# Kernel tuning notes

Hardware: AMD Instinct MI355X
Metric: run time of the kernel (lower is better)

Reference implementation:

```python
import jax, jax.numpy as jnp
import numpy as np

N_AUTHOR, N_FOS, N_INST, N_PAPER = 100000, 30000, 8000, 200000
D_IN, D_OUT = 128, 128
# (name, n_src, n_dst, n_edges)
RELS = [("aff", N_AUTHOR, N_INST, 150000), ("ita", N_INST, N_AUTHOR, 150000),
        ("writes", N_AUTHOR, N_PAPER, 500000), ("pta", N_PAPER, N_AUTHOR, 500000),
        ("cites", N_PAPER, N_PAPER, 1000000), ("topic", N_PAPER, N_FOS, 500000),
        ("ftp", N_FOS, N_PAPER, 500000)]
NODE_SIZES = {"author": N_AUTHOR, "fos": N_FOS, "inst": N_INST, "paper": N_PAPER}


def setup_inputs() -> dict:
    key = jax.random.key(0)
    ks = iter(jax.random.split(key, 64))
    inp = {}
    for nt, n in NODE_SIZES.items():
        inp[f"x_{nt}"] = jax.random.normal(next(ks), (n, D_IN), jnp.float32)
    for name, ns, nd, e in RELS:
        inp[f"src_{name}"] = jax.random.randint(next(ks), (e,), 0, ns, jnp.int64)
        inp[f"dst_{name}"] = jax.random.randint(next(ks), (e,), 0, nd, jnp.int64)
    w_scale = 1.0 / np.sqrt(D_IN)
    for nt in NODE_SIZES:
        inp[f"W_root_{nt}"] = jax.random.uniform(next(ks), (D_IN, D_OUT), jnp.float32, -w_scale, w_scale)
        inp[f"b_root_{nt}"] = jax.random.uniform(next(ks), (D_OUT,), jnp.float32, -w_scale, w_scale)
    for name, _, _, _ in RELS:
        inp[f"W_{name}"] = jax.random.uniform(next(ks), (D_IN, D_OUT), jnp.float32, -w_scale, w_scale)
    return inp


def _mean_agg(x_src, src, dst, n_dst):
    # gather source features along edges, mean-reduce into destinations
    msg = x_src[src]                                             # [E, D_IN]
    s = jax.ops.segment_sum(msg, dst, num_segments=n_dst)        # [n_dst, D_IN]
    cnt = jax.ops.segment_sum(jnp.ones_like(dst, dtype=x_src.dtype), dst, num_segments=n_dst)
    return s / jnp.maximum(cnt, 1.0)[:, None]                    # isolated nodes -> 0


def reference(x_author, x_fos, x_inst, x_paper,
              W_root_author, b_root_author, W_root_fos, b_root_fos,
              W_root_inst, b_root_inst, W_root_paper, b_root_paper,
              W_aff, W_ita, W_writes, W_pta, W_cites, W_topic, W_ftp,
              src_aff, dst_aff, src_ita, dst_ita, src_writes, dst_writes,
              src_pta, dst_pta, src_cites, dst_cites, src_topic, dst_topic,
              src_ftp, dst_ftp):
    # root (self) transforms
    out_author = x_author @ W_root_author + b_root_author
    out_fos = x_fos @ W_root_fos + b_root_fos
    out_inst = x_inst @ W_root_inst + b_root_inst
    out_paper = x_paper @ W_root_paper + b_root_paper
    # per-relation aggregate -> linear -> accumulate into destination type
    out_inst = out_inst + _mean_agg(x_author, src_aff, dst_aff, N_INST) @ W_aff
    out_author = out_author + _mean_agg(x_inst, src_ita, dst_ita, N_AUTHOR) @ W_ita
    out_paper = out_paper + _mean_agg(x_author, src_writes, dst_writes, N_PAPER) @ W_writes
    out_author = out_author + _mean_agg(x_paper, src_pta, dst_pta, N_AUTHOR) @ W_pta
    out_paper = out_paper + _mean_agg(x_paper, src_cites, dst_cites, N_PAPER) @ W_cites
    out_fos = out_fos + _mean_agg(x_paper, src_topic, dst_topic, N_FOS) @ W_topic
    out_paper = out_paper + _mean_agg(x_fos, src_ftp, dst_ftp, N_PAPER) @ W_ftp
    # concatenate per-type outputs (author, fos, inst, paper) along node axis
    return jnp.concatenate([out_author, out_fos, out_inst, out_paper], axis=0)
```

## Files before the change

kernel.cpp:

```cpp
#include <hip/hip_runtime.h>

#define N_AUTHOR 100000
#define N_FOS    30000
#define N_INST   8000
#define N_PAPER  200000
#define NCNT     838000
#define ETOT     3300000

typedef __attribute__((ext_vector_type(8))) short short8v;
typedef __attribute__((ext_vector_type(4))) float float4v;

__device__ __forceinline__ unsigned short f2bf(float f) {
  unsigned u = __float_as_uint(f);
  u = u + 0x7fffu + ((u >> 16) & 1u);
  return (unsigned short)(u >> 16);
}
#define BF2F(s) __uint_as_float(((unsigned)(unsigned short)(s)) << 16)

__device__ __forceinline__ void acc8(float4v& x, float4v& y, short8v h) {
  x[0] += BF2F(h[0]); x[1] += BF2F(h[1]); x[2] += BF2F(h[2]); x[3] += BF2F(h[3]);
  y[0] += BF2F(h[4]); y[1] += BF2F(h[5]); y[2] += BF2F(h[6]); y[3] += BF2F(h[7]);
}

__device__ __forceinline__ short8v pack8(float4v a, float4v b) {
  short8v h;
  h[0] = (short)f2bf(a[0]); h[1] = (short)f2bf(a[1]);
  h[2] = (short)f2bf(a[2]); h[3] = (short)f2bf(a[3]);
  h[4] = (short)f2bf(b[0]); h[5] = (short)f2bf(b[1]);
  h[6] = (short)f2bf(b[2]); h[7] = (short)f2bf(b[3]);
  return h;
}

#define O_CNT    0
#define O_OFFS   3352000
#define O_CURSOR 6704000
#define O_BTOT   10056000
#define O_CSR    10060096
#define O_WT     23260096
#define XB_AUTHOR 23620544
#define XB_FOS    49220544
#define XB_INST   56900544
#define XB_PAPER  58948544
#define WS_NEED_BF 110148544ULL

struct RelTab { const int* src; const int* dst; int E; int base; };
struct Rels { RelTab r[7]; };
struct WPtrs { const float* w[11]; };
struct XCvt { const float* x; unsigned short* xb; int n8; };

__global__ void prep(WPtrs P, unsigned short* __restrict__ wt,
                     int* __restrict__ cnt, XCvt x0, XCvt x1, XCvt x2, XCvt x3,
                     Rels R, int doX) {
  int gsz = gridDim.x * blockDim.x;
  int gtid = blockIdx.x * blockDim.x + threadIdx.x;
  for (int i = gtid; i < 11 * 16384; i += gsz) {
    int mat = i >> 14, rem = i & 16383;
    int k = rem >> 7, n = rem & 127;
    wt[mat * 16384 + n * 128 + k] = f2bf(P.w[mat][rem]);
  }
  if (doX) {
    XCvt xc[4] = {x0, x1, x2, x3};
    #pragma unroll
    for (int a = 0; a < 4; ++a) {
      const float* xp = xc[a].x;
      short8v* xbp = (short8v*)xc[a].xb;
      int n8 = xc[a].n8;
      for (int i = gtid; i < n8; i += gsz) {
        float4v v0 = *(const float4v*)(xp + (size_t)i * 8);
        float4v v1 = *(const float4v*)(xp + (size_t)i * 8 + 4);
        xbp[i] = pack8(v0, v1);
      }
    }
  }
  #pragma unroll
  for (int rr = 0; rr < 7; ++rr) {
    const int* dst = R.r[rr].dst;
    int E = R.r[rr].E, base = R.r[rr].base;
    for (int e = gtid; e < E; e += gsz) atomicAdd(&cnt[base + dst[e]], 1);
  }
}

__global__ void scan1(const int* __restrict__ cnt, int* __restrict__ offs,
                      int* __restrict__ btot, int n) {
  __shared__ int sh[256];
  int tid = threadIdx.x;
  int base = blockIdx.x * 2048 + tid * 8;
  int v[8]; int s = 0;
  #pragma unroll
  for (int i = 0; i < 8; ++i) { v[i] = (base + i < n) ? cnt[base + i] : 0; s += v[i]; }
  sh[tid] = s; __syncthreads();
  for (int off = 1; off < 256; off <<= 1) {
    int t = (tid >= off) ? sh[tid - off] : 0;
    __syncthreads();
    sh[tid] += t;
    __syncthreads();
  }
  int excl = sh[tid] - s;
  if (tid == 255) btot[blockIdx.x] = sh[255];
  int run = excl;
  #pragma unroll
  for (int i = 0; i < 8; ++i) { if (base + i < n) offs[base + i] = run; run += v[i]; }
}

__global__ void scan23(int* __restrict__ offs, int* __restrict__ cursor,
                       const int* __restrict__ btot, int nb, int n) {
  __shared__ int sh[512];
  int tid = threadIdx.x;
  int v = (tid < nb) ? btot[tid] : 0;
  sh[tid] = v; __syncthreads();
  for (int off = 1; off < 512; off <<= 1) {
    int t = (tid >= off) ? sh[tid - off] : 0;
    __syncthreads();
    sh[tid] += t;
    __syncthreads();
  }
  int excl = sh[tid] - v;
  __syncthreads();
  sh[tid] = excl;
  __syncthreads();
  int gsz = gridDim.x * 512;
  for (int idx = blockIdx.x * 512 + tid; idx < n; idx += gsz) {
    int val = offs[idx] + sh[idx >> 11];
    offs[idx] = val;
    cursor[idx] = val;
  }
}

__global__ void fill_k(Rels R, int* __restrict__ cursor, int* __restrict__ csr) {
  int gsz = gridDim.x * blockDim.x;
  int gtid = blockIdx.x * blockDim.x + threadIdx.x;
  #pragma unroll
  for (int rr = 0; rr < 7; ++rr) {
    const int* src = R.r[rr].src;
    const int* dst = R.r[rr].dst;
    int E = R.r[rr].E, base = R.r[rr].base;
    for (int e = gtid; e < E; e += gsz) {
      int p = atomicAdd(&cursor[base + dst[e]], 1);
      __builtin_nontemporal_store(src[e], &csr[p]);
    }
  }
}

template <int NSRC>
__global__ __launch_bounds__(256, 4) void fused_t(
    const unsigned short* __restrict__ x0, const unsigned short* __restrict__ x1,
    const unsigned short* __restrict__ x2, const unsigned short* __restrict__ x3,
    const unsigned short* __restrict__ w0, const unsigned short* __restrict__ w1,
    const unsigned short* __restrict__ w2, const unsigned short* __restrict__ w3,
    int b1, int b2, int b3,
    const int* __restrict__ offs, const int* __restrict__ cnt,
    const int* __restrict__ csr,
    const float* __restrict__ bias, float* __restrict__ out, int n) {
  const int lane = threadIdx.x & 63;
  const int wv = threadIdx.x >> 6;
  const int rb = blockIdx.x * 64 + wv * 16;
  int ar = rb + (lane & 15); if (ar >= n) ar = n - 1;
  const int ch = lane >> 4;
  const int cw = ch * 8;

  const unsigned short* xs[4] = {x0, x1, x2, x3};
  const unsigned short* wsp[4] = {w0, w1, w2, w3};
  const int bases[4] = {0, b1, b2, b3};

  float4v acc[8];
  #pragma unroll
  for (int i = 0; i < 8; ++i) acc[i] = (float4v)0.0f;

  #pragma unroll
  for (int kb = 0; kb < NSRC; ++kb) {
    short8v af[4];
    if (kb == 0) {
      const unsigned short* rp = xs[0] + (size_t)ar * 128 + cw;
      #pragma unroll
      for (int ks = 0; ks < 4; ++ks)
        af[ks] = *(const short8v*)(rp + ks * 32);
    } else {
      int gd = bases[kb] + ar;
      int st = offs[gd];
      int deg = cnt[gd];
      const unsigned short* xb = xs[kb];
      float4v a0[4], a1[4];
      #pragma unroll
      for (int ks = 0; ks < 4; ++ks) { a0[ks] = (float4v)0.f; a1[ks] = (float4v)0.f; }
      int j = 0;
      for (; j + 2 <= deg; j += 2) {
        int s0 = csr[st + j], s1 = csr[st + j + 1];
        const unsigned short* p0 = xb + (size_t)s0 * 128 + cw;
        const unsigned short* p1 = xb + (size_t)s1 * 128 + cw;
        #pragma unroll
        for (int ks = 0; ks < 4; ++ks) {
          short8v h0 = *(const short8v*)(p0 + ks * 32);
          short8v h1 = *(const short8v*)(p1 + ks * 32);
          acc8(a0[ks], a1[ks], h0);
          acc8(a0[ks], a1[ks], h1);
        }
      }
      if (j < deg) {
        int s0 = csr[st + j];
        const unsigned short* p0 = xb + (size_t)s0 * 128 + cw;
        #pragma unroll
        for (int ks = 0; ks < 4; ++ks) {
          short8v h0 = *(const short8v*)(p0 + ks * 32);
          acc8(a0[ks], a1[ks], h0);
        }
      }
      float sc = 1.0f / (float)((deg > 0) ? deg : 1);
      #pragma unroll
      for (int ks = 0; ks < 4; ++ks)
        af[ks] = pack8(a0[ks] * sc, a1[ks] * sc);
    }
    const unsigned short* wb = wsp[kb] + (size_t)(lane & 15) * 128 + cw;
    #pragma unroll
    for (int ct = 0; ct < 8; ++ct) {
      short8v bfr[4];
      #pragma unroll
      for (int ks = 0; ks < 4; ++ks)
        bfr[ks] = *(const short8v*)(wb + ct * 2048 + ks * 32);
      #pragma unroll
      for (int ks = 0; ks < 4; ++ks)
        acc[ct] = __builtin_amdgcn_mfma_f32_16x16x32_bf16(af[ks], bfr[ks], acc[ct], 0, 0, 0);
    }
  }
  #pragma unroll
  for (int ct = 0; ct < 8; ++ct) {
    #pragma unroll
    for (int i = 0; i < 4; ++i) {
      int g = rb + (lane >> 4) * 4 + i;
      if (g < n) {
        int col = ct * 16 + (lane & 15);
        out[(size_t)g * 128 + col] = acc[ct][i] + bias[col];
      }
    }
  }
}

typedef float4v f4;
__global__ __launch_bounds__(256, 4) void fb_gemm(
    const float* __restrict__ x0, const float* __restrict__ x1,
    const float* __restrict__ x2, const float* __restrict__ x3,
    const unsigned short* __restrict__ w0, const unsigned short* __restrict__ w1,
    const unsigned short* __restrict__ w2, const unsigned short* __restrict__ w3,
    int nsrc, int b1, int b2, int b3,
    const int* __restrict__ offs, const int* __restrict__ cnt,
    const int* __restrict__ csr,
    const float* __restrict__ bias, float* __restrict__ out, int n) {
  const int lane = threadIdx.x & 63;
  const int wv = threadIdx.x >> 6;
  const int rb = blockIdx.x * 64 + wv * 16;
  int ar = rb + (lane & 15); if (ar >= n) ar = n - 1;
  const int ch = lane >> 4, cw = ch * 8;
  const float* xs[4] = {x0, x1, x2, x3};
  const unsigned short* wsp[4] = {w0, w1, w2, w3};
  const int bases[4] = {0, b1, b2, b3};
  float4v acc[8];
  #pragma unroll
  for (int i = 0; i < 8; ++i) acc[i] = (float4v)0.0f;
  for (int kb = 0; kb < nsrc; ++kb) {
    short8v af[4];
    const float* xb = xs[kb];
    if (kb == 0) {
      const float* rp = xb + (size_t)ar * 128 + cw;
      #pragma unroll
      for (int ks = 0; ks < 4; ++ks) {
        f4 u = *(const f4*)(rp + ks * 32);
        f4 v = *(const f4*)(rp + ks * 32 + 4);
        af[ks] = pack8(u, v);
      }
    } else {
      int gd = bases[kb] + ar;
      int st = offs[gd];
      int deg = cnt[gd];
      f4 a0[4], a1[4];
      #pragma unroll
      for (int ks = 0; ks < 4; ++ks) { a0[ks] = (f4)0.f; a1[ks] = (f4)0.f; }
      for (int j = 0; j < deg; ++j) {
        int s0 = csr[st + j];
        const float* p0 = xb + (size_t)s0 * 128 + cw;
        #pragma unroll
        for (int ks = 0; ks < 4; ++ks) {
          a0[ks] += *(const f4*)(p0 + ks * 32);
          a1[ks] += *(const f4*)(p0 + ks * 32 + 4);
        }
      }
      float sc = 1.0f / (float)((deg > 0) ? deg : 1);
      #pragma unroll
      for (int ks = 0; ks < 4; ++ks)
        af[ks] = pack8(a0[ks] * sc, a1[ks] * sc);
    }
    const unsigned short* wb = wsp[kb] + (size_t)(lane & 15) * 128 + cw;
    #pragma unroll
    for (int ct = 0; ct < 8; ++ct) {
      short8v bfr[4];
      #pragma unroll
      for (int ks = 0; ks < 4; ++ks)
        bfr[ks] = *(const short8v*)(wb + ct * 2048 + ks * 32);
      #pragma unroll
      for (int ks = 0; ks < 4; ++ks)
        acc[ct] = __builtin_amdgcn_mfma_f32_16x16x32_bf16(af[ks], bfr[ks], acc[ct], 0, 0, 0);
    }
  }
  #pragma unroll
  for (int ct = 0; ct < 8; ++ct) {
    #pragma unroll
    for (int i = 0; i < 4; ++i) {
      int g = rb + (lane >> 4) * 4 + i;
      if (g < n) {
        int col = ct * 16 + (lane & 15);
        out[(size_t)g * 128 + col] = acc[ct][i] + bias[col];
      }
    }
  }
}

extern "C" void kernel_launch(void* const* d_in, const int* in_sizes, int n_in,
                              void* d_out, int out_size, void* d_ws, size_t ws_size,
                              hipStream_t stream) {
  const float* x_author = (const float*)d_in[0];
  const float* x_fos    = (const float*)d_in[1];
  const float* x_inst   = (const float*)d_in[2];
  const float* x_paper  = (const float*)d_in[3];

  Rels R;
  const int E[7]  = {150000, 150000, 500000, 500000, 1000000, 500000, 500000};
  const int ND[7] = {N_INST, N_AUTHOR, N_PAPER, N_AUTHOR, N_PAPER, N_FOS, N_PAPER};
  int base = 0;
  for (int r = 0; r < 7; ++r) {
    R.r[r].src = (const int*)d_in[4 + 2 * r];
    R.r[r].dst = (const int*)d_in[5 + 2 * r];
    R.r[r].E = E[r];
    R.r[r].base = base;
    base += ND[r];
  }

  char* ws = (char*)d_ws;
  int* cnt    = (int*)(ws + O_CNT);
  int* offs   = (int*)(ws + O_OFFS);
  int* cursor = (int*)(ws + O_CURSOR);
  int* btot   = (int*)(ws + O_BTOT);
  int* csr    = (int*)(ws + O_CSR);
  unsigned short* wt = (unsigned short*)(ws + O_WT);
  unsigned short* xbA = (unsigned short*)(ws + XB_AUTHOR);
  unsigned short* xbF = (unsigned short*)(ws + XB_FOS);
  unsigned short* xbI = (unsigned short*)(ws + XB_INST);
  unsigned short* xbP = (unsigned short*)(ws + XB_PAPER);

  const int useBF = (ws_size >= WS_NEED_BF) ? 1 : 0;

  WPtrs WP;
  WP.w[0] = (const float*)d_in[18];
  WP.w[1] = (const float*)d_in[20];
  WP.w[2] = (const float*)d_in[22];
  WP.w[3] = (const float*)d_in[24];
  for (int r = 0; r < 7; ++r) WP.w[4 + r] = (const float*)d_in[26 + r];

  XCvt xcA = {x_author, xbA, N_AUTHOR * 16};
  XCvt xcF = {x_fos,    xbF, N_FOS * 16};
  XCvt xcI = {x_inst,   xbI, N_INST * 16};
  XCvt xcP = {x_paper,  xbP, N_PAPER * 16};

  hipMemsetAsync(cnt, 0, (size_t)NCNT * 4, stream);
  prep<<<2048, 256, 0, stream>>>(WP, wt, cnt, xcA, xcF, xcI, xcP, R, useBF);
  scan1<<<410, 256, 0, stream>>>(cnt, offs, btot, NCNT);
  scan23<<<1024, 512, 0, stream>>>(offs, cursor, btot, 410, NCNT);
  fill_k<<<2048, 256, 0, stream>>>(R, cursor, csr);

  float* out = (float*)d_out;
  const int B_AFF = 0, B_ITA = 8000, B_WRITES = 108000, B_PTA = 308000,
            B_CITES = 408000, B_TOPIC = 608000, B_FTP = 638000;

  const int NB_AUTHOR = (N_AUTHOR + 63) / 64;
  const int NB_FOS    = (N_FOS + 63) / 64;
  const int NB_INST   = (N_INST + 63) / 64;
  const int NB_PAPER  = (N_PAPER + 63) / 64;

  float* outA = out;
  float* outF = out + (size_t)100000 * 128;
  float* outI = out + (size_t)130000 * 128;
  float* outP = out + (size_t)138000 * 128;
  const float* bA = (const float*)d_in[19];
  const float* bF = (const float*)d_in[21];
  const float* bI = (const float*)d_in[23];
  const float* bP = (const float*)d_in[25];

  if (useBF) {
    fused_t<3><<<NB_AUTHOR, 256, 0, stream>>>(
        xbA, xbI, xbP, nullptr,
        wt + 0 * 16384, wt + 5 * 16384, wt + 7 * 16384, nullptr,
        B_ITA, B_PTA, 0, offs, cnt, csr, bA, outA, N_AUTHOR);
    fused_t<2><<<NB_FOS, 256, 0, stream>>>(
        xbF, xbP, nullptr, nullptr,
        wt + 1 * 16384, wt + 9 * 16384, nullptr, nullptr,
        B_TOPIC, 0, 0, offs, cnt, csr, bF, outF, N_FOS);
    fused_t<2><<<NB_INST, 256, 0, stream>>>(
        xbI, xbA, nullptr, nullptr,
        wt + 2 * 16384, wt + 4 * 16384, nullptr, nullptr,
        B_AFF, 0, 0, offs, cnt, csr, bI, outI, N_INST);
    fused_t<4><<<NB_PAPER, 256, 0, stream>>>(
        xbP, xbA, xbP, xbF,
        wt + 3 * 16384, wt + 6 * 16384, wt + 8 * 16384, wt + 10 * 16384,
        B_WRITES, B_CITES, B_FTP, offs, cnt, csr, bP, outP, N_PAPER);
  } else {
    fb_gemm<<<NB_AUTHOR, 256, 0, stream>>>(
        x_author, x_inst, x_paper, nullptr,
        wt + 0 * 16384, wt + 5 * 16384, wt + 7 * 16384, nullptr,
        3, B_ITA, B_PTA, 0, offs, cnt, csr, bA, outA, N_AUTHOR);
    fb_gemm<<<NB_FOS, 256, 0, stream>>>(
        x_fos, x_paper, nullptr, nullptr,
        wt + 1 * 16384, wt + 9 * 16384, nullptr, nullptr,
        2, B_TOPIC, 0, 0, offs, cnt, csr, bF, outF, N_FOS);
    fb_gemm<<<NB_INST, 256, 0, stream>>>(
        x_inst, x_author, nullptr, nullptr,
        wt + 2 * 16384, wt + 4 * 16384, nullptr, nullptr,
        2, B_AFF, 0, 0, offs, cnt, csr, bI, outI, N_INST);
    fb_gemm<<<NB_PAPER, 256, 0, stream>>>(
        x_paper, x_author, x_paper, x_fos,
        wt + 3 * 16384, wt + 6 * 16384, wt + 8 * 16384, wt + 10 * 16384,
        4, B_WRITES, B_CITES, B_FTP, offs, cnt, csr, bP, outP, N_PAPER);
  }
}
```

Before: 979.3 us.

## Merge per-type fused kernels into one launch, unroll gather by four

Replaces the four per-node-type fused gather+GEMM launches with a single kernel that picks the node type from the block index. The heaviest paper blocks come first so the work balances across the device and the tail of each launch is removed. It also unrolls the neighbor gather loop from 2 to 4 edges to keep more loads in flight, raises the occupancy hint to 6 blocks per CU, and writes outputs with nontemporal stores. The cost is higher register pressure from the wider unroll under a tighter launch bound, which could cause spills, plus branch divergence at block level.

```diff
diff --git a/kernel.cpp b/kernel.cpp
--- a/kernel.cpp
+++ b/kernel.cpp
@@ -7,15 +7,30 @@
 #define NCNT     838000
 #define ETOT     3300000
 
+#define NBA 1563
+#define NBF 469
+#define NBI 125
+#define NBP 3125
+#define NB_TOTAL (NBP + NBA + NBF + NBI)
+
+#define B_AFF    0
+#define B_ITA    8000
+#define B_WRITES 108000
+#define B_PTA    308000
+#define B_CITES  408000
+#define B_TOPIC  608000
+#define B_FTP    638000
+
 typedef __attribute__((ext_vector_type(8))) short short8v;
 typedef __attribute__((ext_vector_type(4))) float float4v;
-
-__device__ __forceinline__ unsigned short f2bf(float f) {
+typedef unsigned short us;
+
+__device__ __forceinline__ us f2bf(float f) {
   unsigned u = __float_as_uint(f);
   u = u + 0x7fffu + ((u >> 16) & 1u);
-  return (unsigned short)(u >> 16);
-}
-#define BF2F(s) __uint_as_float(((unsigned)(unsigned short)(s)) << 16)
+  return (us)(u >> 16);
+}
+#define BF2F(s) __uint_as_float(((unsigned)(us)(s)) << 16)
 
 __device__ __forceinline__ void acc8(float4v& x, float4v& y, short8v h) {
   x[0] += BF2F(h[0]); x[1] += BF2F(h[1]); x[2] += BF2F(h[2]); x[3] += BF2F(h[3]);
@@ -46,9 +61,9 @@
 struct RelTab { const int* src; const int* dst; int E; int base; };
 struct Rels { RelTab r[7]; };
 struct WPtrs { const float* w[11]; };
-struct XCvt { const float* x; unsigned short* xb; int n8; };
-
-__global__ void prep(WPtrs P, unsigned short* __restrict__ wt,
+struct XCvt { const float* x; us* xb; int n8; };
+
+__global__ void prep(WPtrs P, us* __restrict__ wt,
                      int* __restrict__ cnt, XCvt x0, XCvt x1, XCvt x2, XCvt x3,
                      Rels R, int doX) {
   int gsz = gridDim.x * blockDim.x;
@@ -142,24 +157,23 @@
 }
 
 template <int NSRC>
-__global__ __launch_bounds__(256, 4) void fused_t(
-    const unsigned short* __restrict__ x0, const unsigned short* __restrict__ x1,
-    const unsigned short* __restrict__ x2, const unsigned short* __restrict__ x3,
-    const unsigned short* __restrict__ w0, const unsigned short* __restrict__ w1,
-    const unsigned short* __restrict__ w2, const unsigned short* __restrict__ w3,
+__device__ __forceinline__ void fused_body(
+    const us* __restrict__ x0, const us* __restrict__ x1,
+    const us* __restrict__ x2, const us* __restrict__ x3,
+    const us* __restrict__ w0, const us* __restrict__ w1,
+    const us* __restrict__ w2, const us* __restrict__ w3,
     int b1, int b2, int b3,
     const int* __restrict__ offs, const int* __restrict__ cnt,
     const int* __restrict__ csr,
-    const float* __restrict__ bias, float* __restrict__ out, int n) {
+    const float* __restrict__ bias, float* __restrict__ out, int n, int rb0) {
   const int lane = threadIdx.x & 63;
   const int wv = threadIdx.x >> 6;
-  const int rb = blockIdx.x * 64 + wv * 16;
+  const int rb = rb0 + wv * 16;
   int ar = rb + (lane & 15); if (ar >= n) ar = n - 1;
-  const int ch = lane >> 4;
-  const int cw = ch * 8;
-
-  const unsigned short* xs[4] = {x0, x1, x2, x3};
-  const unsigned short* wsp[4] = {w0, w1, w2, w3};
+  const int cw = (lane >> 4) * 8;
+
+  const us* xs[4] = {x0, x1, x2, x3};
+  const us* wsp[4] = {w0, w1, w2, w3};
   const int bases[4] = {0, b1, b2, b3};
 
   float4v acc[8];
@@ -170,7 +184,7 @@
   for (int kb = 0; kb < NSRC; ++kb) {
     short8v af[4];
     if (kb == 0) {
-      const unsigned short* rp = xs[0] + (size_t)ar * 128 + cw;
+      const us* rp = xs[0] + (size_t)ar * 128 + cw;
       #pragma unroll
       for (int ks = 0; ks < 4; ++ks)
         af[ks] = *(const short8v*)(rp + ks * 32);
@@ -178,26 +192,33 @@
       int gd = bases[kb] + ar;
       int st = offs[gd];
       int deg = cnt[gd];
-      const unsigned short* xb = xs[kb];
+      const us* xb = xs[kb];
       float4v a0[4], a1[4];
       #pragma unroll
       for (int ks = 0; ks < 4; ++ks) { a0[ks] = (float4v)0.f; a1[ks] = (float4v)0.f; }
       int j = 0;
-      for (; j + 2 <= deg; j += 2) {
-        int s0 = csr[st + j], s1 = csr[st + j + 1];
-        const unsigned short* p0 = xb + (size_t)s0 * 128 + cw;
-        const unsigned short* p1 = xb + (size_t)s1 * 128 + cw;
+      for (; j + 4 <= deg; j += 4) {
+        int s0 = csr[st + j],     s1 = csr[st + j + 1];
+        int s2 = csr[st + j + 2], s3 = csr[st + j + 3];
+        const us* p0 = xb + (size_t)s0 * 128 + cw;
+        const us* p1 = xb + (size_t)s1 * 128 + cw;
+        const us* p2 = xb + (size_t)s2 * 128 + cw;
+        const us* p3 = xb + (size_t)s3 * 128 + cw;
         #pragma unroll
         for (int ks = 0; ks < 4; ++ks) {
           short8v h0 = *(const short8v*)(p0 + ks * 32);
           short8v h1 = *(const short8v*)(p1 + ks * 32);
+          short8v h2 = *(const short8v*)(p2 + ks * 32);
+          short8v h3 = *(const short8v*)(p3 + ks * 32);
           acc8(a0[ks], a1[ks], h0);
           acc8(a0[ks], a1[ks], h1);
+          acc8(a0[ks], a1[ks], h2);
+          acc8(a0[ks], a1[ks], h3);
         }
       }
-      if (j < deg) {
+      for (; j < deg; ++j) {
         int s0 = csr[st + j];
-        const unsigned short* p0 = xb + (size_t)s0 * 128 + cw;
+        const us* p0 = xb + (size_t)s0 * 128 + cw;
         #pragma unroll
         for (int ks = 0; ks < 4; ++ks) {
           short8v h0 = *(const short8v*)(p0 + ks * 32);
@@ -209,7 +230,7 @@
       for (int ks = 0; ks < 4; ++ks)
         af[ks] = pack8(a0[ks] * sc, a1[ks] * sc);
     }
-    const unsigned short* wb = wsp[kb] + (size_t)(lane & 15) * 128 + cw;
+    const us* wb = wsp[kb] + (size_t)(lane & 15) * 128 + cw;
     #pragma unroll
     for (int ct = 0; ct < 8; ++ct) {
       short8v bfr[4];
@@ -228,9 +249,43 @@
       int g = rb + (lane >> 4) * 4 + i;
       if (g < n) {
         int col = ct * 16 + (lane & 15);
-        out[(size_t)g * 128 + col] = acc[ct][i] + bias[col];
-      }
-    }
+        __builtin_nontemporal_store(acc[ct][i] + bias[col],
+                                    &out[(size_t)g * 128 + col]);
+      }
+    }
+  }
+}
+
+__global__ __launch_bounds__(256, 6) void fused_all(
+    const us* __restrict__ xbA, const us* __restrict__ xbF,
+    const us* __restrict__ xbI, const us* __restrict__ xbP,
+    const us* __restrict__ wt,
+    const int* __restrict__ offs, const int* __restrict__ cnt,
+    const int* __restrict__ csr,
+    const float* __restrict__ bA, const float* __restrict__ bF,
+    const float* __restrict__ bI, const float* __restrict__ bP,
+    float* __restrict__ out) {
+  const int bid = blockIdx.x;
+  if (bid < NBP) {
+    fused_body<4>(xbP, xbA, xbP, xbF,
+                  wt + 3 * 16384, wt + 6 * 16384, wt + 8 * 16384, wt + 10 * 16384,
+                  B_WRITES, B_CITES, B_FTP, offs, cnt, csr,
+                  bP, out + (size_t)138000 * 128, N_PAPER, bid * 64);
+  } else if (bid < NBP + NBA) {
+    fused_body<3>(xbA, xbI, xbP, nullptr,
+                  wt + 0 * 16384, wt + 5 * 16384, wt + 7 * 16384, nullptr,
+                  B_ITA, B_PTA, 0, offs, cnt, csr,
+                  bA, out, N_AUTHOR, (bid - NBP) * 64);
+  } else if (bid < NBP + NBA + NBF) {
+    fused_body<2>(xbF, xbP, nullptr, nullptr,
+                  wt + 1 * 16384, wt + 9 * 16384, nullptr, nullptr,
+                  B_TOPIC, 0, 0, offs, cnt, csr,
+                  bF, out + (size_t)100000 * 128, N_FOS, (bid - NBP - NBA) * 64);
+  } else {
+    fused_body<2>(xbI, xbA, nullptr, nullptr,
+                  wt + 2 * 16384, wt + 4 * 16384, nullptr, nullptr,
+                  B_AFF, 0, 0, offs, cnt, csr,
+                  bI, out + (size_t)130000 * 128, N_INST, (bid - NBP - NBA - NBF) * 64);
   }
 }
 
@@ -238,8 +293,8 @@
 __global__ __launch_bounds__(256, 4) void fb_gemm(
     const float* __restrict__ x0, const float* __restrict__ x1,
     const float* __restrict__ x2, const float* __restrict__ x3,
-    const unsigned short* __restrict__ w0, const unsigned short* __restrict__ w1,
-    const unsigned short* __restrict__ w2, const unsigned short* __restrict__ w3,
+    const us* __restrict__ w0, const us* __restrict__ w1,
+    const us* __restrict__ w2, const us* __restrict__ w3,
     int nsrc, int b1, int b2, int b3,
     const int* __restrict__ offs, const int* __restrict__ cnt,
     const int* __restrict__ csr,
@@ -248,9 +303,9 @@
   const int wv = threadIdx.x >> 6;
   const int rb = blockIdx.x * 64 + wv * 16;
   int ar = rb + (lane & 15); if (ar >= n) ar = n - 1;
-  const int ch = lane >> 4, cw = ch * 8;
+  const int cw = (lane >> 4) * 8;
   const float* xs[4] = {x0, x1, x2, x3};
-  const unsigned short* wsp[4] = {w0, w1, w2, w3};
+  const us* wsp[4] = {w0, w1, w2, w3};
   const int bases[4] = {0, b1, b2, b3};
   float4v acc[8];
   #pragma unroll
@@ -287,7 +342,7 @@
       for (int ks = 0; ks < 4; ++ks)
         af[ks] = pack8(a0[ks] * sc, a1[ks] * sc);
     }
-    const unsigned short* wb = wsp[kb] + (size_t)(lane & 15) * 128 + cw;
+    const us* wb = wsp[kb] + (size_t)(lane & 15) * 128 + cw;
     #pragma unroll
     for (int ct = 0; ct < 8; ++ct) {
       short8v bfr[4];
@@ -338,11 +393,11 @@
   int* cursor = (int*)(ws + O_CURSOR);
   int* btot   = (int*)(ws + O_BTOT);
   int* csr    = (int*)(ws + O_CSR);
-  unsigned short* wt = (unsigned short*)(ws + O_WT);
-  unsigned short* xbA = (unsigned short*)(ws + XB_AUTHOR);
-  unsigned short* xbF = (unsigned short*)(ws + XB_FOS);
-  unsigned short* xbI = (unsigned short*)(ws + XB_INST);
-  unsigned short* xbP = (unsigned short*)(ws + XB_PAPER);
+  us* wt  = (us*)(ws + O_WT);
+  us* xbA = (us*)(ws + XB_AUTHOR);
+  us* xbF = (us*)(ws + XB_FOS);
+  us* xbI = (us*)(ws + XB_INST);
+  us* xbP = (us*)(ws + XB_PAPER);
 
   const int useBF = (ws_size >= WS_NEED_BF) ? 1 : 0;
 
@@ -365,56 +420,32 @@
   fill_k<<<2048, 256, 0, stream>>>(R, cursor, csr);
 
   float* out = (float*)d_out;
-  const int B_AFF = 0, B_ITA = 8000, B_WRITES = 108000, B_PTA = 308000,
-            B_CITES = 408000, B_TOPIC = 608000, B_FTP = 638000;
-
-  const int NB_AUTHOR = (N_AUTHOR + 63) / 64;
-  const int NB_FOS    = (N_FOS + 63) / 64;
-  const int NB_INST   = (N_INST + 63) / 64;
-  const int NB_PAPER  = (N_PAPER + 63) / 64;
-
-  float* outA = out;
-  float* outF = out + (size_t)100000 * 128;
-  float* outI = out + (size_t)130000 * 128;
-  float* outP = out + (size_t)138000 * 128;
   const float* bA = (const float*)d_in[19];
   const float* bF = (const float*)d_in[21];
   const float* bI = (const float*)d_in[23];
   const float* bP = (const float*)d_in[25];
 
   if (useBF) {
-    fused_t<3><<<NB_AUTHOR, 256, 0, stream>>>(
-        xbA, xbI, xbP, nullptr,
-        wt + 0 * 16384, wt + 5 * 16384, wt + 7 * 16384, nullptr,
-        B_ITA, B_PTA, 0, offs, cnt, csr, bA, outA, N_AUTHOR);
-    fused_t<2><<<NB_FOS, 256, 0, stream>>>(
-        xbF, xbP, nullptr, nullptr,
-        wt + 1 * 16384, wt + 9 * 16384, nullptr, nullptr,
-        B_TOPIC, 0, 0, offs, cnt, csr, bF, outF, N_FOS);
-    fused_t<2><<<NB_INST, 256, 0, stream>>>(
-        xbI, xbA, nullptr, nullptr,
-        wt + 2 * 16384, wt + 4 * 16384, nullptr, nullptr,
-        B_AFF, 0, 0, offs, cnt, csr, bI, outI, N_INST);
-    fused_t<4><<<NB_PAPER, 256, 0, stream>>>(
-        xbP, xbA, xbP, xbF,
-        wt + 3 * 16384, wt + 6 * 16384, wt + 8 * 16384, wt + 10 * 16384,
-        B_WRITES, B_CITES, B_FTP, offs, cnt, csr, bP, outP, N_PAPER);
+    fused_all<<<NB_TOTAL, 256, 0, stream>>>(xbA, xbF, xbI, xbP, wt,
+                                            offs, cnt, csr,
+                                            bA, bF, bI, bP, out);
   } else {
-    fb_gemm<<<NB_AUTHOR, 256, 0, stream>>>(
+    fb_gemm<<<NBA, 256, 0, stream>>>(
         x_author, x_inst, x_paper, nullptr,
         wt + 0 * 16384, wt + 5 * 16384, wt + 7 * 16384, nullptr,
-        3, B_ITA, B_PTA, 0, offs, cnt, csr, bA, outA, N_AUTHOR);
-    fb_gemm<<<NB_FOS, 256, 0, stream>>>(
+        3, B_ITA, B_PTA, 0, offs, cnt, csr, bA, out, N_AUTHOR);
+    fb_gemm<<<NBF, 256, 0, stream>>>(
         x_fos, x_paper, nullptr, nullptr,
         wt + 1 * 16384, wt + 9 * 16384, nullptr, nullptr,
-        2, B_TOPIC, 0, 0, offs, cnt, csr, bF, outF, N_FOS);
-    fb_gemm<<<NB_INST, 256, 0, stream>>>(
+        2, B_TOPIC, 0, 0, offs, cnt, csr, bF, out + (size_t)100000 * 128, N_FOS);
+    fb_gemm<<<NBI, 256, 0, stream>>>(
         x_inst, x_author, nullptr, nullptr,
         wt + 2 * 16384, wt + 4 * 16384, nullptr, nullptr,
-        2, B_AFF, 0, 0, offs, cnt, csr, bI, outI, N_INST);
-    fb_gemm<<<NB_PAPER, 256, 0, stream>>>(
+        2, B_AFF, 0, 0, offs, cnt, csr, bI, out + (size_t)130000 * 128, N_INST);
+    fb_gemm<<<NBP, 256, 0, stream>>>(
         x_paper, x_author, x_paper, x_fos,
         wt + 3 * 16384, wt + 6 * 16384, wt + 8 * 16384, wt + 10 * 16384,
-        4, B_WRITES, B_CITES, B_FTP, offs, cnt, csr, bP, outP, N_PAPER);
-  }
-}
+        4, B_WRITES, B_CITES, B_FTP, offs, cnt, csr, bP,
+        out + (size_t)138000 * 128, N_PAPER);
+  }
+}
```

Result: faster. 928.6 us (-5.2%).
